# Performance work log

Hardware: AMD Instinct MI355X
Metric: run time of the kernel (lower is better)

The kernel has to match this reference:

```python
import jax, jax.numpy as jnp
import numpy as np

IN_OCT = 512
OUT_OCT = 512
BATCH = 512


def setup_inputs() -> dict:
    key = jax.random.key(0)
    kx, kw = jax.random.split(key)
    x = jax.random.normal(kx, (BATCH, IN_OCT * 8), dtype=jnp.float32)
    weight = jax.random.normal(kw, (OUT_OCT, IN_OCT, 8, 8), dtype=jnp.float32)
    bias = jnp.zeros((OUT_OCT, 8), dtype=jnp.float32)
    return {"x": x, "weight": weight, "bias": bias}


def reference(x, weight, bias):
    # x: [B, in_oct*8]; weight: [out_oct, in_oct, 8, 8]; bias: [out_oct, 8]
    B = x.shape[0]
    out_oct, in_oct = weight.shape[0], weight.shape[1]
    xo = x.reshape(B, in_oct, 8)
    # octonion_mul(x[:, j], weight[i, j]) applies the per-pair 8x8 octonion
    # left-multiplication matrix; summed over j it is one bilinear contraction.
    y = jnp.einsum("bjp,ijpk->bik", xo, weight) + bias[None, :, :]
    return y.reshape(B, out_oct * 8)
```

## Files before the change

### kernel.cpp

```cpp
#include <hip/hip_runtime.h>
#include <stdint.h>


#define M_DIM 512
#define N_DIM 4096
#define K_DIM 4096
#define KSPLIT 4

typedef __bf16 bf16x8 __attribute__((ext_vector_type(8)));
typedef float f32x4 __attribute__((ext_vector_type(4)));

__device__ inline unsigned short f2bf(float f) {
  union { float f; unsigned int u; } v;
  v.f = f;
  unsigned int u = v.u;
  unsigned int r = (u + 0x7fffu + ((u >> 16) & 1u)) >> 16;
  return (unsigned short)r;
}

__global__ __launch_bounds__(256) void prep_kernel(
    const float* __restrict__ x, const float* __restrict__ w,
    const float* __restrict__ bias, unsigned short* __restrict__ abf,
    unsigned short* __restrict__ bt, float* __restrict__ out) {
  const int bid = blockIdx.x;
  const int t = threadIdx.x;
  if (bid < 4096) {
    __shared__ __align__(16) unsigned short lT[8][512];
    const int i = bid >> 3;
    const int jg = bid & 7;
    const float4* src =
        (const float4*)(w + (size_t)i * 32768 + jg * 4096 + t * 16);
    float4 v0 = src[0], v1 = src[1], v2 = src[2], v3 = src[3];
    const int jp = (t >> 2) * 8 + (t & 3) * 2;
    unsigned int* dst32;
    const float* lo = (const float*)&v0;
    const float* hi = (const float*)&v2;
#pragma unroll
    for (int k = 0; k < 4; ++k) {
      unsigned int pk =
          (unsigned int)f2bf(lo[k]) | ((unsigned int)f2bf(hi[k]) << 16);
      *(unsigned int*)&lT[k][jp] = pk;
    }
    lo = (const float*)&v1;
    hi = (const float*)&v3;
#pragma unroll
    for (int k = 0; k < 4; ++k) {
      unsigned int pk =
          (unsigned int)f2bf(lo[k]) | ((unsigned int)f2bf(hi[k]) << 16);
      *(unsigned int*)&lT[k + 4][jp] = pk;
    }
    __syncthreads();
    const int r = t >> 5, c = t & 31;
    const uint4* s = (const uint4*)&lT[r][c * 16];
    uint4* d = (uint4*)(bt + (size_t)(i * 8 + r) * K_DIM + jg * 512 + c * 16);
    d[0] = s[0];
    d[1] = s[1];
  } else if (bid < 5120) {
    int g = (bid - 4096) * 256 + t;
    const float4* xi = (const float4*)x;
    float4 a = xi[g * 2];
    float4 b = xi[g * 2 + 1];
    __attribute__((aligned(16))) unsigned short o[8] = {
        f2bf(a.x), f2bf(a.y), f2bf(a.z), f2bf(a.w),
        f2bf(b.x), f2bf(b.y), f2bf(b.z), f2bf(b.w)};
    *(uint4*)(abf + (size_t)g * 8) = *(const uint4*)o;
  } else {
    int g = (bid - 5120) * 256 + t;
    int el = g * 4;
    int col = el & (N_DIM - 1);
    *(float4*)(out + el) = *(const float4*)(bias + col);
  }
}

__device__ inline void gld16(const void* g, void* l) {
  __builtin_amdgcn_global_load_lds(
      (const __attribute__((address_space(1))) unsigned int*)g,
      (__attribute__((address_space(3))) unsigned int*)l, 16, 0, 0);
}

__global__ __launch_bounds__(256) void gemm_kernel(
    const unsigned short* __restrict__ A, const unsigned short* __restrict__ Bt,
    float* __restrict__ out) {
  __shared__ __align__(16) unsigned short lA[2][128 * 32];
  __shared__ __align__(16) unsigned short lB[2][128 * 32];
  const int t = threadIdx.x;
  const int n0 = blockIdx.x * 128;
  const int m0 = blockIdx.y * 128;
  const int kc0 = blockIdx.z * (K_DIM / KSPLIT);
  const int w = t >> 6;
  const int lane = t & 63;
  const int wr = w >> 1;
  const int wc = w & 1;
  const int lrow = lane & 15;
  const int kb = lane >> 4;

  f32x4 acc[4][4] = {};

  const int s0 = t, s1 = t + 256;
  const int row0 = s0 >> 2, c0 = (s0 & 3) * 8;
  const int row1 = s1 >> 2, c1 = (s1 & 3) * 8;
  const size_t aO0 = (size_t)(m0 + row0) * K_DIM + c0;
  const size_t aO1 = (size_t)(m0 + row1) * K_DIM + c1;
  const size_t bO0 = (size_t)(n0 + row0) * K_DIM + c0;
  const size_t bO1 = (size_t)(n0 + row1) * K_DIM + c1;

  const int NIT = (K_DIM / KSPLIT) / 32;

  gld16(A + aO0 + kc0, (char*)lA[0] + s0 * 16);
  gld16(Bt + bO0 + kc0, (char*)lB[0] + s0 * 16);
  gld16(A + aO1 + kc0, (char*)lA[0] + (s1 - 256) * 16 + 4096);
  gld16(Bt + bO1 + kc0, (char*)lB[0] + (s1 - 256) * 16 + 4096);

  for (int it = 0; it < NIT; ++it) {
    __syncthreads();
    if (it + 1 < NIT) {
      const int kk = kc0 + (it + 1) * 32;
      char* dA = (char*)lA[(it + 1) & 1];
      char* dB = (char*)lB[(it + 1) & 1];
      gld16(A + aO0 + kk, dA + s0 * 16);
      gld16(Bt + bO0 + kk, dB + s0 * 16);
      gld16(A + aO1 + kk, dA + (s1 - 256) * 16 + 4096);
      gld16(Bt + bO1 + kk, dB + (s1 - 256) * 16 + 4096);
    }
    const unsigned short* cA = lA[it & 1];
    const unsigned short* cB = lB[it & 1];

    bf16x8 af[4], bfr[4];
#pragma unroll
    for (int mt = 0; mt < 4; ++mt)
      af[mt] = *(const bf16x8*)(cA + (wr * 64 + mt * 16 + lrow) * 32 + kb * 8);
#pragma unroll
    for (int nt = 0; nt < 4; ++nt)
      bfr[nt] = *(const bf16x8*)(cB + (wc * 64 + nt * 16 + lrow) * 32 + kb * 8);
#pragma unroll
    for (int mt = 0; mt < 4; ++mt)
#pragma unroll
      for (int nt = 0; nt < 4; ++nt)
        acc[mt][nt] = __builtin_amdgcn_mfma_f32_16x16x32_bf16(
            af[mt], bfr[nt], acc[mt][nt], 0, 0, 0);
  }

#pragma unroll
  for (int mt = 0; mt < 4; ++mt) {
    const int gmb = m0 + wr * 64 + mt * 16 + kb * 4;
#pragma unroll
    for (int nt = 0; nt < 4; ++nt) {
      const int gn = n0 + wc * 64 + nt * 16 + lrow;
#pragma unroll
      for (int r = 0; r < 4; ++r)
        atomicAdd(out + (size_t)(gmb + r) * N_DIM + gn, acc[mt][nt][r]);
    }
  }
}

extern "C" void kernel_launch(void* const* d_in, const int* in_sizes, int n_in,
                              void* d_out, int out_size, void* d_ws,
                              size_t ws_size, hipStream_t stream) {
  const float* x = (const float*)d_in[0];
  const float* w = (const float*)d_in[1];
  const float* bias = (const float*)d_in[2];
  float* out = (float*)d_out;

  unsigned short* abf = (unsigned short*)d_ws;
  unsigned short* bt = abf + (size_t)M_DIM * K_DIM;

  prep_kernel<<<7168, 256, 0, stream>>>(x, w, bias, abf, bt, out);

  dim3 grid(N_DIM / 128, M_DIM / 128, KSPLIT);
  gemm_kernel<<<grid, 256, 0, stream>>>(abf, bt, out);
}
```

Before: 155.7 us.

## Give each wave private LDS tiles and replace block barriers with waitcnt

Each wave now loads its own 64-row A and B slices into a private LDS region with async global-to-LDS loads. Per-iteration __syncthreads is replaced by manual s_waitcnt on vmcnt/lgkmcnt, so waves progress independently. The cost is duplicated global traffic, since A and B slices are loaded twice across the waves that share them, and LDS use doubles to 64KB, which may cut occupancy. It also relies on hand-encoded waitcnt values being correct for the gfx target.

```diff
diff --git a/kernel.cpp b/kernel.cpp
--- a/kernel.cpp
+++ b/kernel.cpp
@@ -6,6 +6,7 @@
 #define N_DIM 4096
 #define K_DIM 4096
 #define KSPLIT 4
+#define NIT ((K_DIM / KSPLIT) / 32)
 
 typedef __bf16 bf16x8 __attribute__((ext_vector_type(8)));
 typedef float f32x4 __attribute__((ext_vector_type(4)));
@@ -32,7 +33,6 @@
         (const float4*)(w + (size_t)i * 32768 + jg * 4096 + t * 16);
     float4 v0 = src[0], v1 = src[1], v2 = src[2], v3 = src[3];
     const int jp = (t >> 2) * 8 + (t & 3) * 2;
-    unsigned int* dst32;
     const float* lo = (const float*)&v0;
     const float* hi = (const float*)&v2;
 #pragma unroll
@@ -78,11 +78,14 @@
       (__attribute__((address_space(3))) unsigned int*)l, 16, 0, 0);
 }
 
+#define WAIT_VM8 0x0F78
+#define WAIT_VM0 0x0F70
+#define WAIT_LGKM0 0xC07F
+
 __global__ __launch_bounds__(256) void gemm_kernel(
     const unsigned short* __restrict__ A, const unsigned short* __restrict__ Bt,
     float* __restrict__ out) {
-  __shared__ __align__(16) unsigned short lA[2][128 * 32];
-  __shared__ __align__(16) unsigned short lB[2][128 * 32];
+  __shared__ __align__(16) char lds[4 * 2 * 8192];
   const int t = threadIdx.x;
   const int n0 = blockIdx.x * 128;
   const int m0 = blockIdx.y * 128;
@@ -93,45 +96,49 @@
   const int wc = w & 1;
   const int lrow = lane & 15;
   const int kb = lane >> 4;
+  char* wbase = lds + w * 16384;
+  char* ldsLane = wbase + lane * 16;
+
+  const int srow = lane >> 2;
+  const int scol = (lane & 3) * 8;
+  const unsigned short* gA0 =
+      A + (size_t)(m0 + wr * 64 + srow) * K_DIM + kc0 + scol;
+  const unsigned short* gB0 =
+      Bt + (size_t)(n0 + wc * 64 + srow) * K_DIM + kc0 + scol;
 
   f32x4 acc[4][4] = {};
 
-  const int s0 = t, s1 = t + 256;
-  const int row0 = s0 >> 2, c0 = (s0 & 3) * 8;
-  const int row1 = s1 >> 2, c1 = (s1 & 3) * 8;
-  const size_t aO0 = (size_t)(m0 + row0) * K_DIM + c0;
-  const size_t aO1 = (size_t)(m0 + row1) * K_DIM + c1;
-  const size_t bO0 = (size_t)(n0 + row0) * K_DIM + c0;
-  const size_t bO1 = (size_t)(n0 + row1) * K_DIM + c1;
+  auto issue = [&](int it) {
+    char* dA = ldsLane + (it & 1) * 8192;
+    char* dB = dA + 4096;
+    const unsigned short* gA = gA0 + it * 32;
+    const unsigned short* gB = gB0 + it * 32;
+#pragma unroll
+    for (int q = 0; q < 4; ++q) {
+      gld16(gA + (size_t)q * 16 * K_DIM, dA + q * 1024);
+      gld16(gB + (size_t)q * 16 * K_DIM, dB + q * 1024);
+    }
+  };
 
-  const int NIT = (K_DIM / KSPLIT) / 32;
-
-  gld16(A + aO0 + kc0, (char*)lA[0] + s0 * 16);
-  gld16(Bt + bO0 + kc0, (char*)lB[0] + s0 * 16);
-  gld16(A + aO1 + kc0, (char*)lA[0] + (s1 - 256) * 16 + 4096);
-  gld16(Bt + bO1 + kc0, (char*)lB[0] + (s1 - 256) * 16 + 4096);
-
+  issue(0);
   for (int it = 0; it < NIT; ++it) {
-    __syncthreads();
     if (it + 1 < NIT) {
-      const int kk = kc0 + (it + 1) * 32;
-      char* dA = (char*)lA[(it + 1) & 1];
-      char* dB = (char*)lB[(it + 1) & 1];
-      gld16(A + aO0 + kk, dA + s0 * 16);
-      gld16(Bt + bO0 + kk, dB + s0 * 16);
-      gld16(A + aO1 + kk, dA + (s1 - 256) * 16 + 4096);
-      gld16(Bt + bO1 + kk, dB + (s1 - 256) * 16 + 4096);
+      __builtin_amdgcn_s_waitcnt(WAIT_LGKM0);
+      issue(it + 1);
+      __builtin_amdgcn_s_waitcnt(WAIT_VM8);
+    } else {
+      __builtin_amdgcn_s_waitcnt(WAIT_VM0);
     }
-    const unsigned short* cA = lA[it & 1];
-    const unsigned short* cB = lB[it & 1];
+    const unsigned short* cA = (const unsigned short*)(wbase + (it & 1) * 8192);
+    const unsigned short* cB = cA + 2048;
 
     bf16x8 af[4], bfr[4];
 #pragma unroll
     for (int mt = 0; mt < 4; ++mt)
-      af[mt] = *(const bf16x8*)(cA + (wr * 64 + mt * 16 + lrow) * 32 + kb * 8);
+      af[mt] = *(const bf16x8*)(cA + (mt * 16 + lrow) * 32 + kb * 8);
 #pragma unroll
     for (int nt = 0; nt < 4; ++nt)
-      bfr[nt] = *(const bf16x8*)(cB + (wc * 64 + nt * 16 + lrow) * 32 + kb * 8);
+      bfr[nt] = *(const bf16x8*)(cB + (nt * 16 + lrow) * 32 + kb * 8);
 #pragma unroll
     for (int mt = 0; mt < 4; ++mt)
 #pragma unroll
```

After: 155.6 us. No clear change (-0.0%).

## Load GEMM fragments directly from global memory into registers, dropping LDS staging

Applied to the files above, without the earlier changes.

The GEMM kernel no longer stages A and B tiles through double-buffered shared memory with global_load_lds. Each wave now loads its own MFMA fragments straight from global memory into a register double buffer, with the K loop fully unrolled and launch bounds raised to ask for two blocks per CU. This removes the LDS round trip and the per-iteration barrier. In exchange, fragments that waves share are no longer reused within the block, so each wave makes its own narrow 16-byte strided global loads, and the extra registers may limit occupancy.

```diff
diff --git a/kernel.cpp b/kernel.cpp
--- a/kernel.cpp
+++ b/kernel.cpp
@@ -6,6 +6,7 @@
 #define N_DIM 4096
 #define K_DIM 4096
 #define KSPLIT 4
+#define NIT ((K_DIM / KSPLIT) / 32)
 
 typedef __bf16 bf16x8 __attribute__((ext_vector_type(8)));
 typedef float f32x4 __attribute__((ext_vector_type(4)));
@@ -32,7 +33,6 @@
         (const float4*)(w + (size_t)i * 32768 + jg * 4096 + t * 16);
     float4 v0 = src[0], v1 = src[1], v2 = src[2], v3 = src[3];
     const int jp = (t >> 2) * 8 + (t & 3) * 2;
-    unsigned int* dst32;
     const float* lo = (const float*)&v0;
     const float* hi = (const float*)&v2;
 #pragma unroll
@@ -72,17 +72,9 @@
   }
 }
 
-__device__ inline void gld16(const void* g, void* l) {
-  __builtin_amdgcn_global_load_lds(
-      (const __attribute__((address_space(1))) unsigned int*)g,
-      (__attribute__((address_space(3))) unsigned int*)l, 16, 0, 0);
-}
-
-__global__ __launch_bounds__(256) void gemm_kernel(
+__global__ __launch_bounds__(256, 2) void gemm_kernel(
     const unsigned short* __restrict__ A, const unsigned short* __restrict__ Bt,
     float* __restrict__ out) {
-  __shared__ __align__(16) unsigned short lA[2][128 * 32];
-  __shared__ __align__(16) unsigned short lB[2][128 * 32];
   const int t = threadIdx.x;
   const int n0 = blockIdx.x * 128;
   const int m0 = blockIdx.y * 128;
@@ -94,50 +86,41 @@
   const int lrow = lane & 15;
   const int kb = lane >> 4;
 
+  const unsigned short* pA[4];
+  const unsigned short* pB[4];
+#pragma unroll
+  for (int mt = 0; mt < 4; ++mt)
+    pA[mt] = A + (size_t)(m0 + wr * 64 + mt * 16 + lrow) * K_DIM + kc0 + kb * 8;
+#pragma unroll
+  for (int nt = 0; nt < 4; ++nt)
+    pB[nt] =
+        Bt + (size_t)(n0 + wc * 64 + nt * 16 + lrow) * K_DIM + kc0 + kb * 8;
+
   f32x4 acc[4][4] = {};
+  bf16x8 fA[2][4], fB[2][4];
 
-  const int s0 = t, s1 = t + 256;
-  const int row0 = s0 >> 2, c0 = (s0 & 3) * 8;
-  const int row1 = s1 >> 2, c1 = (s1 & 3) * 8;
-  const size_t aO0 = (size_t)(m0 + row0) * K_DIM + c0;
-  const size_t aO1 = (size_t)(m0 + row1) * K_DIM + c1;
-  const size_t bO0 = (size_t)(n0 + row0) * K_DIM + c0;
-  const size_t bO1 = (size_t)(n0 + row1) * K_DIM + c1;
+#pragma unroll
+  for (int mt = 0; mt < 4; ++mt) {
+    fA[0][mt] = *(const bf16x8*)(pA[mt]);
+    fB[0][mt] = *(const bf16x8*)(pB[mt]);
+  }
 
-  const int NIT = (K_DIM / KSPLIT) / 32;
-
-  gld16(A + aO0 + kc0, (char*)lA[0] + s0 * 16);
-  gld16(Bt + bO0 + kc0, (char*)lB[0] + s0 * 16);
-  gld16(A + aO1 + kc0, (char*)lA[0] + (s1 - 256) * 16 + 4096);
-  gld16(Bt + bO1 + kc0, (char*)lB[0] + (s1 - 256) * 16 + 4096);
-
+#pragma unroll
   for (int it = 0; it < NIT; ++it) {
-    __syncthreads();
+    const int cur = it & 1, nxt = cur ^ 1;
     if (it + 1 < NIT) {
-      const int kk = kc0 + (it + 1) * 32;
-      char* dA = (char*)lA[(it + 1) & 1];
-      char* dB = (char*)lB[(it + 1) & 1];
-      gld16(A + aO0 + kk, dA + s0 * 16);
-      gld16(Bt + bO0 + kk, dB + s0 * 16);
-      gld16(A + aO1 + kk, dA + (s1 - 256) * 16 + 4096);
-      gld16(Bt + bO1 + kk, dB + (s1 - 256) * 16 + 4096);
+#pragma unroll
+      for (int mt = 0; mt < 4; ++mt) {
+        fA[nxt][mt] = *(const bf16x8*)(pA[mt] + (it + 1) * 32);
+        fB[nxt][mt] = *(const bf16x8*)(pB[mt] + (it + 1) * 32);
+      }
     }
-    const unsigned short* cA = lA[it & 1];
-    const unsigned short* cB = lB[it & 1];
-
-    bf16x8 af[4], bfr[4];
-#pragma unroll
-    for (int mt = 0; mt < 4; ++mt)
-      af[mt] = *(const bf16x8*)(cA + (wr * 64 + mt * 16 + lrow) * 32 + kb * 8);
-#pragma unroll
-    for (int nt = 0; nt < 4; ++nt)
-      bfr[nt] = *(const bf16x8*)(cB + (wc * 64 + nt * 16 + lrow) * 32 + kb * 8);
 #pragma unroll
     for (int mt = 0; mt < 4; ++mt)
 #pragma unroll
       for (int nt = 0; nt < 4; ++nt)
         acc[mt][nt] = __builtin_amdgcn_mfma_f32_16x16x32_bf16(
-            af[mt], bfr[nt], acc[mt][nt], 0, 0, 0);
+            fA[cur][mt], fB[cur][nt], acc[mt][nt], 0, 0, 0);
   }
 
 #pragma unroll
```

New measurement: 183.2 us. +17.7%, slower.
